# Performance work log

Hardware: AMD Instinct MI355X
Metric: run time of the kernel (lower is better)

Reference implementation:

```python
import jax, jax.numpy as jnp
import numpy as np

N_NODES = 50000
N_EDGES = 800000
IN_DIM = 13
HID = 64
LAYER_DIMS = [(IN_DIM, HID), (HID, HID), (HID, HID), (HID, HID), (HID, 1)]


def setup_inputs() -> dict:
    key = jax.random.key(0)
    ks = jax.random.split(key, 20)
    x = jax.random.normal(ks[0], (N_NODES, IN_DIM), dtype=jnp.float32)
    edge_index = jax.random.randint(ks[1], (2, N_EDGES), 0, N_NODES)
    edge_weight = jax.random.uniform(ks[2], (N_EDGES,), dtype=jnp.float32)
    inp = {"x": x, "edge_index": edge_index, "edge_weight": edge_weight}
    for i, (di, do) in enumerate(LAYER_DIMS):
        s = 1.0 / np.sqrt(di)
        inp[f"Wrel{i}"] = (jax.random.normal(ks[3 + 3 * i], (di, do)) * s).astype(jnp.float32)
        inp[f"brel{i}"] = jnp.zeros((do,), dtype=jnp.float32)
        inp[f"Wroot{i}"] = (jax.random.normal(ks[4 + 3 * i], (di, do)) * s).astype(jnp.float32)
    return inp


def _graph_conv(x, src, dst, ew, Wrel, brel, Wroot):
    # PyG GraphConv: out = lin_rel(sum_{j in N(i)} w_e * x_j) + lin_root(x_i)
    msgs = ew[:, None] * x[src]                      # [E, d_in] gather
    aggr = jax.ops.segment_sum(msgs, dst, num_segments=N_NODES)  # [N, d_in]
    return aggr @ Wrel + brel + x @ Wroot


def reference(x, edge_index, edge_weight,
              Wrel0, brel0, Wroot0,
              Wrel1, brel1, Wroot1,
              Wrel2, brel2, Wroot2,
              Wrel3, brel3, Wroot3,
              Wrel4, brel4, Wroot4):
    src, dst = edge_index[0], edge_index[1]  # source_to_target flow
    params = [
        (Wrel0, brel0, Wroot0),
        (Wrel1, brel1, Wroot1),
        (Wrel2, brel2, Wroot2),
        (Wrel3, brel3, Wroot3),
        (Wrel4, brel4, Wroot4),
    ]
    h = x
    for Wr, br, Ws in params[:-1]:
        h = jax.nn.relu(_graph_conv(h, src, dst, edge_weight, Wr, br, Ws))
    Wr, br, Ws = params[-1]
    h = _graph_conv(h, src, dst, edge_weight, Wr, br, Ws)
    return jax.nn.sigmoid(h)  # [N, 1]
```

## Files before the change

### kernel.cpp

```cpp
#include <hip/hip_runtime.h>
#include <math.h>

#define N_NODES 50000
#define N_EDGES 800000
#define NBUCKET 196
#define CHUNK 4096
#define NCHUNK 196
#define SCAN_N (NBUCKET * NCHUNK)
#define SB_A 151
#define SB_B 196
#define NSB (SB_A + SB_B)
#define EPT 16
#define CAP_FINE 8192
#define MAXEPAD (N_EDGES + N_NODES * 4)
#define XELEMS (N_NODES * 13)
#define XCONV_B 32

typedef __attribute__((ext_vector_type(8))) _Float16 f16x8;
typedef __attribute__((ext_vector_type(4))) float f32x4;

__device__ __forceinline__ int roundup4(int v) { return (v + 3) & ~3; }


__device__ __forceinline__ int block_excl_scan(int v, int* wsum) {
    int t = threadIdx.x, lane = t & 63, w = t >> 6;
    int sc = v;
    #pragma unroll
    for (int o = 1; o < 64; o <<= 1) {
        int u = __shfl_up(sc, o, 64);
        if (lane >= o) sc += u;
    }
    if (lane == 63) wsum[w] = sc;
    __syncthreads();
    int add = 0;
    #pragma unroll
    for (int j = 0; j < 4; ++j) if (j < w) add += wsum[j];
    return add + sc - v;
}


__global__ void hist_kernel(const int* __restrict__ dst, int* __restrict__ h,
                            int* __restrict__ counts,
                            const float* __restrict__ W1r, const float* __restrict__ W1o,
                            const float* __restrict__ W2r, const float* __restrict__ W2o,
                            const float* __restrict__ W3r, const float* __restrict__ W3o,
                            _Float16* __restrict__ wfrag,
                            const float* __restrict__ x, _Float16* __restrict__ xh) {
    if (blockIdx.x >= NCHUNK + 3) {
        int b = blockIdx.x - (NCHUNK + 3);
        for (int i = b * 256 + threadIdx.x; i < XELEMS; i += XCONV_B * 256)
            xh[i] = (_Float16)x[i];
        return;
    }
    if (blockIdx.x >= NCHUNK) {
        int b = blockIdx.x - NCHUNK, t = threadIdx.x;
        const float* Wr = (b == 0) ? W1r : (b == 1) ? W2r : W3r;
        const float* Wo = (b == 0) ? W1o : (b == 1) ? W2o : W3o;
        _Float16* out = wfrag + (size_t)b * 8192;
        for (int i = t; i < 1024; i += 256) {
            int frag = i >> 6, lane = i & 63;
            int m = frag >> 3, ct = (frag >> 1) & 3, ks = frag & 1;
            int col = ct * 16 + (lane & 15);
            int kb = ks * 32 + (lane >> 4) * 8;
            const float* W = m ? Wo : Wr;
            f16x8 v;
            #pragma unroll
            for (int j = 0; j < 8; ++j) v[j] = (_Float16)W[(kb + j) * 64 + col];
            *(f16x8*)&out[(size_t)i * 8] = v;
        }
        return;
    }
    __shared__ int hist[NBUCKET];
    for (int i = threadIdx.x; i < NBUCKET; i += 256) hist[i] = 0;
    __syncthreads();
    int base = blockIdx.x * CHUNK;
    int n = min(CHUNK, N_EDGES - base);
    for (int k = threadIdx.x; k < n; k += 256) {
        int d = dst[base + k];
        atomicAdd(&hist[d >> 8], 1);
        atomicAdd(&counts[d], 1);
    }
    __syncthreads();
    for (int i = threadIdx.x; i < NBUCKET; i += 256)
        h[i * NCHUNK + blockIdx.x] = hist[i];
}


__global__ void scan_sums(const int* __restrict__ h, const int* __restrict__ counts,
                          int* __restrict__ blocksums) {
    __shared__ int wsum[4];
    int bid = blockIdx.x, t = threadIdx.x;
    int v;
    if (bid < SB_A) {
        int i = bid * 256 + t;
        v = (i < SCAN_N) ? h[i] : 0;
    } else {
        int j = (bid - SB_A) * 256 + t;
        v = (j < N_NODES) ? roundup4(counts[j]) : 0;
    }
    int lane = t & 63, w = t >> 6;
    int s = v;
    #pragma unroll
    for (int o = 1; o < 64; o <<= 1) s += __shfl_xor(s, o, 64);
    if (lane == 0) wsum[w] = s;
    __syncthreads();
    if (t == 0) blocksums[bid] = wsum[0] + wsum[1] + wsum[2] + wsum[3];
}

__global__ void scan_apply(int* __restrict__ h, int* __restrict__ offs,
                           const int* __restrict__ counts,
                           const int* __restrict__ blocksums) {
    __shared__ int sblk[NSB + 1];
    __shared__ int wsum[4];
    int bid = blockIdx.x, t = threadIdx.x;
    if (t < 64) {
        int carry = 0;
        for (int c = 0; c < NSB; c += 64) {
            int i = c + t;
            int v = (i < NSB) ? blocksums[i] : 0;
            int sc = v;
            #pragma unroll
            for (int o = 1; o < 64; o <<= 1) {
                int u = __shfl_up(sc, o, 64);
                if (t >= o) sc += u;
            }
            if (i < NSB) sblk[i] = carry + sc - v;
            carry += __shfl(sc, 63, 64);
        }
        if (t == 0) sblk[NSB] = carry;
    }
    __syncthreads();
    int v;
    if (bid < SB_A) {
        int i = bid * 256 + t;
        v = (i < SCAN_N) ? h[i] : 0;
        int e = block_excl_scan(v, wsum);
        int base = sblk[bid];
        if (i < SCAN_N) h[i] = e + base;
    } else {
        int j = (bid - SB_A) * 256 + t;
        v = (j < N_NODES) ? roundup4(counts[j]) : 0;
        int e = block_excl_scan(v, wsum);
        int base = sblk[bid] - sblk[SB_A];
        if (j < N_NODES) {
            offs[j] = e + base;
            if (j == N_NODES - 1) offs[N_NODES] = e + base + v;
        }
    }
}


__launch_bounds__(256, 4)
__global__ void scatter_coarse(const int* __restrict__ src, const int* __restrict__ dst,
                               const float* __restrict__ ew, const int* __restrict__ hs,
                               int2* __restrict__ ecoarse) {
    __shared__ int cnt[NBUCKET];
    __shared__ int excl[NBUCKET];
    __shared__ int cur[NBUCKET];
    __shared__ int gbase[NBUCKET];
    __shared__ int wsum[4];
    __shared__ int2 stage[CHUNK];

    int t = threadIdx.x;
    int base = blockIdx.x * CHUNK;
    int n = min(CHUNK, N_EDGES - base);

    for (int i = t; i < NBUCKET; i += 256) {
        cnt[i] = 0;
        gbase[i] = hs[i * NCHUNK + blockIdx.x];
    }
    __syncthreads();

    int rx[EPT];
    float rw[EPT];
    #pragma unroll
    for (int j = 0; j < EPT; ++j) {
        int k = t + j * 256;
        if (k < n) {
            int e = base + k;
            int d = dst[e];
            rx[j] = (d << 16) | src[e];
            rw[j] = ew[e];
            atomicAdd(&cnt[d >> 8], 1);
        }
    }
    __syncthreads();

    {
        int v = (t < NBUCKET) ? cnt[t] : 0;
        int e = block_excl_scan(v, wsum);
        if (t < NBUCKET) { excl[t] = e; cur[t] = e; }
    }
    __syncthreads();

    #pragma unroll
    for (int j = 0; j < EPT; ++j) {
        int k = t + j * 256;
        if (k < n) {
            int b = ((unsigned)rx[j]) >> 24;
            int p = atomicAdd(&cur[b], 1);
            stage[p] = make_int2(rx[j], __float_as_int(rw[j]));
        }
    }
    __syncthreads();

    for (int k = t; k < n; k += 256) {
        int2 r = stage[k];
        int b = ((unsigned)r.x) >> 24;
        ecoarse[gbase[b] + (k - excl[b])] = r;
    }
}


__launch_bounds__(256)
__global__ void fine_sort(const int* __restrict__ h, const int* __restrict__ offs,
                          const int2* __restrict__ ecoarse, int2* __restrict__ esrt) {
    int b = blockIdx.x, t = threadIdx.x;
    __shared__ int cur[256];
    __shared__ int2 stage[CAP_FINE];
    int bstartU = h[b * NCHUNK];
    int bendU = (b == NBUCKET - 1) ? N_EDGES : h[(b + 1) * NCHUNK];
    int nbU = bendU - bstartU;
    int P = offs[b << 8];
    int nodeEnd = min((b + 1) << 8, N_NODES);
    int plen = offs[nodeEnd] - P;
    int dstv = (b << 8) + t;
    cur[t] = (dstv < N_NODES) ? offs[dstv] - P : 0;
    __syncthreads();
    if (plen <= CAP_FINE) {
        for (int k = t; k < plen; k += 256) stage[k] = make_int2(0, 0);
        __syncthreads();
        for (int k = t; k < nbU; k += 256) {
            int2 r = ecoarse[bstartU + k];
            int d = (((unsigned)r.x) >> 16) & 255;
            int p = atomicAdd(&cur[d], 1);
            stage[p] = make_int2(r.x & 0xFFFF, r.y);
        }
        __syncthreads();
        for (int k = t; k < plen; k += 256) esrt[P + k] = stage[k];
    } else {
        for (int k = t; k < plen; k += 256) esrt[P + k] = make_int2(0, 0);
        __syncthreads();
        for (int k = t; k < nbU; k += 256) {
            int2 r = ecoarse[bstartU + k];
            int d = (((unsigned)r.x) >> 16) & 255;
            int p = atomicAdd(&cur[d], 1);
            esrt[P + p] = make_int2(r.x & 0xFFFF, r.y);
        }
    }
}


__device__ __forceinline__ float bcast(float v, int k) {
    return __int_as_float(__builtin_amdgcn_readlane(__float_as_int(v), k));
}


__launch_bounds__(256)
__global__ void layer0_fused(const int* __restrict__ offs, const int2* __restrict__ esrt,
                             const _Float16* __restrict__ xh, const float* __restrict__ Wrel,
                             const float* __restrict__ bias, const float* __restrict__ Wroot,
                             _Float16* __restrict__ h0) {
    int wid = (blockIdx.x * blockDim.x + threadIdx.x) >> 6;
    int lane = threadIdx.x & 63;
    float wr[13], wo[13];
    #pragma unroll
    for (int k = 0; k < 13; ++k) {
        wr[k] = Wrel[k * 64 + lane];
        wo[k] = Wroot[k * 64 + lane];
    }
    float bc = bias[lane];
    int q = lane >> 4, f = lane & 15;
    int beg = offs[wid], end = offs[wid + 1];
    float acc = 0.f;
    bool fv = (f < 13);
    int i = beg + q;
    for (; i + 4 < end; i += 8) {
        int2 e0 = esrt[i], e1 = esrt[i + 4];
        float v0 = fv ? (float)xh[(size_t)e0.x * 13 + f] : 0.f;
        float v1 = fv ? (float)xh[(size_t)e1.x * 13 + f] : 0.f;
        acc = fmaf(__int_as_float(e0.y), v0, acc);
        acc = fmaf(__int_as_float(e1.y), v1, acc);
    }
    if (i < end) {
        int2 e = esrt[i];
        float v = fv ? (float)xh[(size_t)e.x * 13 + f] : 0.f;
        acc = fmaf(__int_as_float(e.y), v, acc);
    }
    acc += __shfl_xor(acc, 16, 64);
    acc += __shfl_xor(acc, 32, 64);
    float hv = (lane < 13) ? (float)xh[(size_t)wid * 13 + lane] : 0.f;
    float a0 = bc, a1 = 0.f, a2 = 0.f, a3 = 0.f;
    #pragma unroll
    for (int k = 0; k + 2 <= 13; k += 2) {
        a0 = fmaf(bcast(acc, k), wr[k], a0);
        a1 = fmaf(bcast(hv, k), wo[k], a1);
        a2 = fmaf(bcast(acc, k + 1), wr[k + 1], a2);
        a3 = fmaf(bcast(hv, k + 1), wo[k + 1], a3);
    }
    a0 = fmaf(bcast(acc, 12), wr[12], a0);
    a1 = fmaf(bcast(hv, 12), wo[12], a1);
    float o = fmaxf((a0 + a2) + (a1 + a3), 0.f);
    h0[(size_t)wid * 64 + lane] = (_Float16)o;
}


template <bool FINAL>
__launch_bounds__(256)
__global__ void layer_fused(const int* __restrict__ offs, const int2* __restrict__ esrt,
                            const _Float16* __restrict__ hin, const _Float16* __restrict__ wfrag_l,
                            const float* __restrict__ bias, _Float16* __restrict__ hout,
                            const float* __restrict__ Wrel4, const float* __restrict__ Wroot4,
                            float* __restrict__ z, float* __restrict__ root) {
    __shared__ __align__(16) _Float16 aggrHi[32][72];
    __shared__ __align__(16) _Float16 aggrLo[32][72];
    __shared__ float zpart[4][32], rpart[4][32];
    int t = threadIdx.x;
    int rowbase = blockIdx.x * 32;
    int w = t >> 6, lane = t & 63;

    f16x8 br0 = *(const f16x8*)&wfrag_l[(size_t)(((0 * 4 + w) * 2 + 0) * 64 + lane) * 8];
    f16x8 br1 = *(const f16x8*)&wfrag_l[(size_t)(((0 * 4 + w) * 2 + 1) * 64 + lane) * 8];
    f16x8 bo0 = *(const f16x8*)&wfrag_l[(size_t)(((1 * 4 + w) * 2 + 0) * 64 + lane) * 8];
    f16x8 bo1 = *(const f16x8*)&wfrag_l[(size_t)(((1 * 4 + w) * 2 + 1) * 64 + lane) * 8];
    int r = lane & 15, kq = lane >> 4;
    float bc = bias[w * 16 + r];
    float w4rv = 0.f, w4ov = 0.f;
    if (FINAL) { w4rv = Wrel4[w * 16 + r]; w4ov = Wroot4[w * 16 + r]; }

    int qw = t >> 4, l = t & 15;
    int hi8 = l >> 3, f8 = l & 7;
    #pragma unroll
    for (int rr = 0; rr < 2; ++rr) {
        int node = rowbase + qw + rr * 16;
        float a[8] = {0.f, 0.f, 0.f, 0.f, 0.f, 0.f, 0.f, 0.f};
        if (node < N_NODES) {
            int beg = offs[node], end = offs[node + 1];
            int i = beg;
            for (; i + 4 < end; i += 8) {
                int4 p0 = *(const int4*)(esrt + i);
                int4 p1 = *(const int4*)(esrt + i + 2);
                int4 p2 = *(const int4*)(esrt + i + 4);
                int4 p3 = *(const int4*)(esrt + i + 6);
                int s0 = hi8 ? p0.z : p0.x; float w0 = __int_as_float(hi8 ? p0.w : p0.y);
                int s1 = hi8 ? p1.z : p1.x; float w1 = __int_as_float(hi8 ? p1.w : p1.y);
                int s2 = hi8 ? p2.z : p2.x; float w2 = __int_as_float(hi8 ? p2.w : p2.y);
                int s3 = hi8 ? p3.z : p3.x; float w3 = __int_as_float(hi8 ? p3.w : p3.y);
                f16x8 r0 = *(const f16x8*)(hin + (size_t)s0 * 64 + f8 * 8);
                f16x8 r1 = *(const f16x8*)(hin + (size_t)s1 * 64 + f8 * 8);
                f16x8 r2 = *(const f16x8*)(hin + (size_t)s2 * 64 + f8 * 8);
                f16x8 r3 = *(const f16x8*)(hin + (size_t)s3 * 64 + f8 * 8);
                #pragma unroll
                for (int j = 0; j < 8; ++j) {
                    a[j] = fmaf(w0, (float)r0[j], a[j]);
                    a[j] = fmaf(w1, (float)r1[j], a[j]);
                    a[j] = fmaf(w2, (float)r2[j], a[j]);
                    a[j] = fmaf(w3, (float)r3[j], a[j]);
                }
            }
            if (i < end) {
                int4 p0 = *(const int4*)(esrt + i);
                int4 p1 = *(const int4*)(esrt + i + 2);
                int s0 = hi8 ? p0.z : p0.x; float w0 = __int_as_float(hi8 ? p0.w : p0.y);
                int s1 = hi8 ? p1.z : p1.x; float w1 = __int_as_float(hi8 ? p1.w : p1.y);
                f16x8 r0 = *(const f16x8*)(hin + (size_t)s0 * 64 + f8 * 8);
                f16x8 r1 = *(const f16x8*)(hin + (size_t)s1 * 64 + f8 * 8);
                #pragma unroll
                for (int j = 0; j < 8; ++j) {
                    a[j] = fmaf(w0, (float)r0[j], a[j]);
                    a[j] = fmaf(w1, (float)r1[j], a[j]);
                }
            }
        }
        #pragma unroll
        for (int j = 0; j < 8; ++j) a[j] += __shfl_xor(a[j], 8, 64);
        f16x8 wv;
        #pragma unroll
        for (int j = 0; j < 8; ++j) {
            _Float16 hh = (_Float16)a[j];
            wv[j] = hi8 ? (_Float16)(a[j] - (float)hh) : hh;
        }
        int row = qw + rr * 16;
        _Float16* dstp = hi8 ? &aggrLo[row][f8 * 8] : &aggrHi[row][f8 * 8];
        *(f16x8*)dstp = wv;
    }
    __syncthreads();

    #pragma unroll
    for (int g = 0; g < 2; ++g) {
        int lr = g * 16 + r;
        int grow = min(rowbase + lr, N_NODES - 1);
        f32x4 acc = {bc, bc, bc, bc};
        {
            f16x8 Ah = *(const f16x8*)&aggrHi[lr][0 * 32 + kq * 8];
            f16x8 Al = *(const f16x8*)&aggrLo[lr][0 * 32 + kq * 8];
            f16x8 Ar = *(const f16x8*)&hin[(size_t)grow * 64 + 0 * 32 + kq * 8];
            acc = __builtin_amdgcn_mfma_f32_16x16x32_f16(Ah, br0, acc, 0, 0, 0);
            acc = __builtin_amdgcn_mfma_f32_16x16x32_f16(Al, br0, acc, 0, 0, 0);
            acc = __builtin_amdgcn_mfma_f32_16x16x32_f16(Ar, bo0, acc, 0, 0, 0);
        }
        {
            f16x8 Ah = *(const f16x8*)&aggrHi[lr][1 * 32 + kq * 8];
            f16x8 Al = *(const f16x8*)&aggrLo[lr][1 * 32 + kq * 8];
            f16x8 Ar = *(const f16x8*)&hin[(size_t)grow * 64 + 1 * 32 + kq * 8];
            acc = __builtin_amdgcn_mfma_f32_16x16x32_f16(Ah, br1, acc, 0, 0, 0);
            acc = __builtin_amdgcn_mfma_f32_16x16x32_f16(Al, br1, acc, 0, 0, 0);
            acc = __builtin_amdgcn_mfma_f32_16x16x32_f16(Ar, bo1, acc, 0, 0, 0);
        }
        if (FINAL) {
            #pragma unroll
            for (int j = 0; j < 4; ++j) {
                float o = fmaxf(acc[j], 0.f);
                float zz = o * w4rv, rv = o * w4ov;
                #pragma unroll
                for (int m = 1; m < 16; m <<= 1) {
                    zz += __shfl_xor(zz, m, 64);
                    rv += __shfl_xor(rv, m, 64);
                }
                if (r == 0) {
                    int lrow = g * 16 + (lane >> 4) * 4 + j;
                    zpart[w][lrow] = zz;
                    rpart[w][lrow] = rv;
                }
            }
        } else {
            #pragma unroll
            for (int j = 0; j < 4; ++j) {
                int row = rowbase + g * 16 + (lane >> 4) * 4 + j;
                if (row < N_NODES)
                    hout[(size_t)row * 64 + w * 16 + r] = (_Float16)fmaxf(acc[j], 0.f);
            }
        }
    }
    if (FINAL) {
        __syncthreads();
        if (t < 32) {
            int row = rowbase + t;
            if (row < N_NODES) {
                z[row] = zpart[0][t] + zpart[1][t] + zpart[2][t] + zpart[3][t];
                root[row] = rpart[0][t] + rpart[1][t] + rpart[2][t] + rpart[3][t];
            }
        }
    }
}


__launch_bounds__(256)
__global__ void final_aggr(const int* __restrict__ offs, const int2* __restrict__ esrt,
                           const float* __restrict__ z, const float* __restrict__ root,
                           const float* __restrict__ b4, float* __restrict__ out) {
    int tid = blockIdx.x * blockDim.x + threadIdx.x;
    int node = tid >> 2, g = tid & 3;
    if (node >= N_NODES) return;
    int beg = offs[node], end = offs[node + 1];
    float a = 0.f;
    int i = beg + g;
    for (; i + 4 < end; i += 8) {
        int2 e0 = esrt[i], e1 = esrt[i + 4];
        a = fmaf(__int_as_float(e0.y), z[e0.x], a);
        a = fmaf(__int_as_float(e1.y), z[e1.x], a);
    }
    if (i < end) {
        int2 e = esrt[i];
        a = fmaf(__int_as_float(e.y), z[e.x], a);
    }
    a += __shfl_xor(a, 1, 64);
    a += __shfl_xor(a, 2, 64);
    if (g == 0) {
        float v = a + b4[0] + root[node];
        out[node] = 1.f / (1.f + expf(-v));
    }
}


extern "C" void kernel_launch(void* const* d_in, const int* in_sizes, int n_in,
                              void* d_out, int out_size, void* d_ws, size_t ws_size,
                              hipStream_t stream) {
    const float* x = (const float*)d_in[0];
    const int* eidx = (const int*)d_in[1];
    const float* ew = (const float*)d_in[2];
    const float* Wrel[5];
    const float* brel[5];
    const float* Wroot[5];
    for (int i = 0; i < 5; ++i) {
        Wrel[i] = (const float*)d_in[3 + 3 * i];
        brel[i] = (const float*)d_in[4 + 3 * i];
        Wroot[i] = (const float*)d_in[5 + 3 * i];
    }
    const int* src = eidx;
    const int* dst = eidx + N_EDGES;
    float* out = (float*)d_out;

    char* ws = (char*)d_ws;
    size_t off = 0;
    auto alloc = [&](size_t bytes) -> void* {
        void* p = ws + off;
        off = (off + bytes + 255) & ~(size_t)255;
        return p;
    };
    int* h = (int*)alloc((size_t)(SCAN_N + 256) * 4);
    int* blocksums = (int*)alloc(512 * 4);
    int* counts = (int*)alloc((size_t)N_NODES * 4);
    int* offs = (int*)alloc((size_t)(N_NODES + 1) * 4);
    int2* esrt = (int2*)alloc((size_t)MAXEPAD * 8);
    _Float16* h0 = (_Float16*)alloc((size_t)N_NODES * 64 * 2);
    _Float16* h1 = (_Float16*)alloc((size_t)N_NODES * 64 * 2);
    _Float16* wfrag = (_Float16*)alloc((size_t)3 * 8192 * 2);
    _Float16* xh = (_Float16*)alloc((size_t)XELEMS * 2);
    float* z = (float*)alloc((size_t)N_NODES * 4);
    float* root = (float*)alloc((size_t)N_NODES * 4);
    int2* ecoarse = (int2*)h0;
    (void)ws_size; (void)in_sizes; (void)n_in; (void)out_size;

    hipMemsetAsync(counts, 0, (size_t)N_NODES * 4, stream);
    hist_kernel<<<NCHUNK + 3 + XCONV_B, 256, 0, stream>>>(dst, h, counts,
                                                Wrel[1], Wroot[1], Wrel[2], Wroot[2],
                                                Wrel[3], Wroot[3], wfrag, x, xh);
    scan_sums<<<NSB, 256, 0, stream>>>(h, counts, blocksums);
    scan_apply<<<NSB, 256, 0, stream>>>(h, offs, counts, blocksums);
    scatter_coarse<<<NCHUNK, 256, 0, stream>>>(src, dst, ew, h, ecoarse);
    fine_sort<<<NBUCKET, 256, 0, stream>>>(h, offs, ecoarse, esrt);

    const int NODE_BLOCKS = N_NODES * 64 / 256;
    const int FB = (N_NODES + 31) / 32;

    layer0_fused<<<NODE_BLOCKS, 256, 0, stream>>>(offs, esrt, xh, Wrel[0], brel[0], Wroot[0], h0);

    layer_fused<false><<<FB, 256, 0, stream>>>(offs, esrt, h0, wfrag, brel[1], h1,
                                               nullptr, nullptr, nullptr, nullptr);
    layer_fused<false><<<FB, 256, 0, stream>>>(offs, esrt, h1, wfrag + 8192, brel[2], h0,
                                               nullptr, nullptr, nullptr, nullptr);
    layer_fused<true><<<FB, 256, 0, stream>>>(offs, esrt, h0, wfrag + 16384, brel[3], nullptr,
                                              Wrel[4], Wroot[4], z, root);

    final_aggr<<<(N_NODES * 4 + 255) / 256, 256, 0, stream>>>(offs, esrt, z, root, brel[4], out);
}
```

Baseline: 180.6 us.

## Pack edges into 32-bit src/fp16 weight and fuse layers via persistent grid barrier

Edge records shrink from an int2 (src, fp32 weight) to one 32-bit word holding a 16-bit source index and an fp16 weight. This halves edge-list traffic in every aggregation pass. Layers 1-3 and the final aggregation are also merged into one persistent kernel that loops over tiles and syncs through a hand-rolled atomic grid barrier, removing three kernel launches. The trade-offs: the weight loses precision in fp16, and the 16-bit index only works because fine_sort stores the low 16 bits with the bucket implied by the destination. The spin barrier can also deadlock if not all blocks are co-resident, which depends on the occupancy query and assumes 256 CUs.

```diff
diff --git a/kernel.cpp b/kernel.cpp
--- a/kernel.cpp
+++ b/kernel.cpp
@@ -15,11 +15,18 @@
 #define MAXEPAD (N_EDGES + N_NODES * 4)
 #define XELEMS (N_NODES * 13)
 #define XCONV_B 32
+#define FB ((N_NODES + 31) / 32)
+#define FINB ((N_NODES * 4 + 255) / 256)
 
 typedef __attribute__((ext_vector_type(8))) _Float16 f16x8;
 typedef __attribute__((ext_vector_type(4))) float f32x4;
 
 __device__ __forceinline__ int roundup4(int v) { return (v + 3) & ~3; }
+
+__device__ __forceinline__ float upw(int e) {
+    unsigned short u = (unsigned short)(((unsigned)e) >> 16);
+    return (float)__builtin_bit_cast(_Float16, u);
+}
 
 
 __device__ __forceinline__ int block_excl_scan(int v, int* wsum) {
@@ -45,7 +52,9 @@
                             const float* __restrict__ W2r, const float* __restrict__ W2o,
                             const float* __restrict__ W3r, const float* __restrict__ W3o,
                             _Float16* __restrict__ wfrag,
-                            const float* __restrict__ x, _Float16* __restrict__ xh) {
+                            const float* __restrict__ x, _Float16* __restrict__ xh,
+                            int* __restrict__ bar) {
+    if (blockIdx.x == 0 && threadIdx.x < 8) bar[threadIdx.x] = 0;
     if (blockIdx.x >= NCHUNK + 3) {
         int b = blockIdx.x - (NCHUNK + 3);
         for (int i = b * 256 + threadIdx.x; i < XELEMS; i += XCONV_B * 256)
@@ -214,10 +223,10 @@
 
 __launch_bounds__(256)
 __global__ void fine_sort(const int* __restrict__ h, const int* __restrict__ offs,
-                          const int2* __restrict__ ecoarse, int2* __restrict__ esrt) {
+                          const int2* __restrict__ ecoarse, int* __restrict__ epack) {
     int b = blockIdx.x, t = threadIdx.x;
     __shared__ int cur[256];
-    __shared__ int2 stage[CAP_FINE];
+    __shared__ int stage[CAP_FINE];
     int bstartU = h[b * NCHUNK];
     int bendU = (b == NBUCKET - 1) ? N_EDGES : h[(b + 1) * NCHUNK];
     int nbU = bendU - bstartU;
@@ -228,24 +237,26 @@
     cur[t] = (dstv < N_NODES) ? offs[dstv] - P : 0;
     __syncthreads();
     if (plen <= CAP_FINE) {
-        for (int k = t; k < plen; k += 256) stage[k] = make_int2(0, 0);
+        for (int k = t; k < plen; k += 256) stage[k] = 0;
         __syncthreads();
         for (int k = t; k < nbU; k += 256) {
             int2 r = ecoarse[bstartU + k];
             int d = (((unsigned)r.x) >> 16) & 255;
+            unsigned short hw = __builtin_bit_cast(unsigned short, (_Float16)__int_as_float(r.y));
             int p = atomicAdd(&cur[d], 1);
-            stage[p] = make_int2(r.x & 0xFFFF, r.y);
+            stage[p] = (r.x & 0xFFFF) | ((int)hw << 16);
         }
         __syncthreads();
-        for (int k = t; k < plen; k += 256) esrt[P + k] = stage[k];
+        for (int k = t; k < plen; k += 256) epack[P + k] = stage[k];
     } else {
-        for (int k = t; k < plen; k += 256) esrt[P + k] = make_int2(0, 0);
+        for (int k = t; k < plen; k += 256) epack[P + k] = 0;
         __syncthreads();
         for (int k = t; k < nbU; k += 256) {
             int2 r = ecoarse[bstartU + k];
             int d = (((unsigned)r.x) >> 16) & 255;
+            unsigned short hw = __builtin_bit_cast(unsigned short, (_Float16)__int_as_float(r.y));
             int p = atomicAdd(&cur[d], 1);
-            esrt[P + p] = make_int2(r.x & 0xFFFF, r.y);
+            epack[P + p] = (r.x & 0xFFFF) | ((int)hw << 16);
         }
     }
 }
@@ -257,7 +268,7 @@
 
 
 __launch_bounds__(256)
-__global__ void layer0_fused(const int* __restrict__ offs, const int2* __restrict__ esrt,
+__global__ void layer0_fused(const int* __restrict__ offs, const int* __restrict__ epack,
                              const _Float16* __restrict__ xh, const float* __restrict__ Wrel,
                              const float* __restrict__ bias, const float* __restrict__ Wroot,
                              _Float16* __restrict__ h0) {
@@ -276,16 +287,16 @@
     bool fv = (f < 13);
     int i = beg + q;
     for (; i + 4 < end; i += 8) {
-        int2 e0 = esrt[i], e1 = esrt[i + 4];
-        float v0 = fv ? (float)xh[(size_t)e0.x * 13 + f] : 0.f;
-        float v1 = fv ? (float)xh[(size_t)e1.x * 13 + f] : 0.f;
-        acc = fmaf(__int_as_float(e0.y), v0, acc);
-        acc = fmaf(__int_as_float(e1.y), v1, acc);
+        int e0 = epack[i], e1 = epack[i + 4];
+        float v0 = fv ? (float)xh[(size_t)(e0 & 0xFFFF) * 13 + f] : 0.f;
+        float v1 = fv ? (float)xh[(size_t)(e1 & 0xFFFF) * 13 + f] : 0.f;
+        acc = fmaf(upw(e0), v0, acc);
+        acc = fmaf(upw(e1), v1, acc);
     }
     if (i < end) {
-        int2 e = esrt[i];
-        float v = fv ? (float)xh[(size_t)e.x * 13 + f] : 0.f;
-        acc = fmaf(__int_as_float(e.y), v, acc);
+        int e = epack[i];
+        float v = fv ? (float)xh[(size_t)(e & 0xFFFF) * 13 + f] : 0.f;
+        acc = fmaf(upw(e), v, acc);
     }
     acc += __shfl_xor(acc, 16, 64);
     acc += __shfl_xor(acc, 32, 64);
@@ -306,17 +317,16 @@
 
 
 template <bool FINAL>
-__launch_bounds__(256)
-__global__ void layer_fused(const int* __restrict__ offs, const int2* __restrict__ esrt,
-                            const _Float16* __restrict__ hin, const _Float16* __restrict__ wfrag_l,
-                            const float* __restrict__ bias, _Float16* __restrict__ hout,
-                            const float* __restrict__ Wrel4, const float* __restrict__ Wroot4,
-                            float* __restrict__ z, float* __restrict__ root) {
-    __shared__ __align__(16) _Float16 aggrHi[32][72];
-    __shared__ __align__(16) _Float16 aggrLo[32][72];
-    __shared__ float zpart[4][32], rpart[4][32];
+__device__ __forceinline__ void layer_tile(
+    int tile, const int* __restrict__ offs, const int* __restrict__ epack,
+    const _Float16* __restrict__ hin, const _Float16* __restrict__ wfrag_l,
+    const float* __restrict__ bias, _Float16* __restrict__ hout,
+    const float* __restrict__ Wrel4, const float* __restrict__ Wroot4,
+    float* __restrict__ z, float* __restrict__ root,
+    _Float16 (*aggrHi)[72], _Float16 (*aggrLo)[72],
+    float (*zpart)[32], float (*rpart)[32]) {
     int t = threadIdx.x;
-    int rowbase = blockIdx.x * 32;
+    int rowbase = tile * 32;
     int w = t >> 6, lane = t & 63;
 
     f16x8 br0 = *(const f16x8*)&wfrag_l[(size_t)(((0 * 4 + w) * 2 + 0) * 64 + lane) * 8];
@@ -338,18 +348,17 @@
             int beg = offs[node], end = offs[node + 1];
             int i = beg;
             for (; i + 4 < end; i += 8) {
-                int4 p0 = *(const int4*)(esrt + i);
-                int4 p1 = *(const int4*)(esrt + i + 2);
-                int4 p2 = *(const int4*)(esrt + i + 4);
-                int4 p3 = *(const int4*)(esrt + i + 6);
-                int s0 = hi8 ? p0.z : p0.x; float w0 = __int_as_float(hi8 ? p0.w : p0.y);
-                int s1 = hi8 ? p1.z : p1.x; float w1 = __int_as_float(hi8 ? p1.w : p1.y);
-                int s2 = hi8 ? p2.z : p2.x; float w2 = __int_as_float(hi8 ? p2.w : p2.y);
-                int s3 = hi8 ? p3.z : p3.x; float w3 = __int_as_float(hi8 ? p3.w : p3.y);
-                f16x8 r0 = *(const f16x8*)(hin + (size_t)s0 * 64 + f8 * 8);
-                f16x8 r1 = *(const f16x8*)(hin + (size_t)s1 * 64 + f8 * 8);
-                f16x8 r2 = *(const f16x8*)(hin + (size_t)s2 * 64 + f8 * 8);
-                f16x8 r3 = *(const f16x8*)(hin + (size_t)s3 * 64 + f8 * 8);
+                int4 pk0 = *(const int4*)(epack + i);
+                int4 pk1 = *(const int4*)(epack + i + 4);
+                int e0 = hi8 ? pk0.z : pk0.x;
+                int e1 = hi8 ? pk0.w : pk0.y;
+                int e2 = hi8 ? pk1.z : pk1.x;
+                int e3 = hi8 ? pk1.w : pk1.y;
+                f16x8 r0 = *(const f16x8*)(hin + (size_t)(e0 & 0xFFFF) * 64 + f8 * 8);
+                f16x8 r1 = *(const f16x8*)(hin + (size_t)(e1 & 0xFFFF) * 64 + f8 * 8);
+                f16x8 r2 = *(const f16x8*)(hin + (size_t)(e2 & 0xFFFF) * 64 + f8 * 8);
+                f16x8 r3 = *(const f16x8*)(hin + (size_t)(e3 & 0xFFFF) * 64 + f8 * 8);
+                float w0 = upw(e0), w1 = upw(e1), w2 = upw(e2), w3 = upw(e3);
                 #pragma unroll
                 for (int j = 0; j < 8; ++j) {
                     a[j] = fmaf(w0, (float)r0[j], a[j]);
@@ -359,12 +368,12 @@
                 }
             }
             if (i < end) {
-                int4 p0 = *(const int4*)(esrt + i);
-                int4 p1 = *(const int4*)(esrt + i + 2);
-                int s0 = hi8 ? p0.z : p0.x; float w0 = __int_as_float(hi8 ? p0.w : p0.y);
-                int s1 = hi8 ? p1.z : p1.x; float w1 = __int_as_float(hi8 ? p1.w : p1.y);
-                f16x8 r0 = *(const f16x8*)(hin + (size_t)s0 * 64 + f8 * 8);
-                f16x8 r1 = *(const f16x8*)(hin + (size_t)s1 * 64 + f8 * 8);
+                int4 pk = *(const int4*)(epack + i);
+                int e0 = hi8 ? pk.z : pk.x;
+                int e1 = hi8 ? pk.w : pk.y;
+                f16x8 r0 = *(const f16x8*)(hin + (size_t)(e0 & 0xFFFF) * 64 + f8 * 8);
+                f16x8 r1 = *(const f16x8*)(hin + (size_t)(e1 & 0xFFFF) * 64 + f8 * 8);
+                float w0 = upw(e0), w1 = upw(e1);
                 #pragma unroll
                 for (int j = 0; j < 8; ++j) {
                     a[j] = fmaf(w0, (float)r0[j], a[j]);
@@ -442,34 +451,82 @@
             }
         }
     }
+    __syncthreads();
+}
+
+
+__device__ __forceinline__ void final_tile(int tile, const int* __restrict__ offs,
+                                           const int* __restrict__ epack,
+                                           const float* __restrict__ z,
+                                           const float* __restrict__ root,
+                                           const float* __restrict__ b4,
+                                           float* __restrict__ out) {
+    int tid = tile * 256 + threadIdx.x;
+    int node = tid >> 2, g = tid & 3;
+    if (node < N_NODES) {
+        int beg = offs[node], end = offs[node + 1];
+        float a = 0.f;
+        int i = beg + g;
+        for (; i + 4 < end; i += 8) {
+            int e0 = epack[i], e1 = epack[i + 4];
+            a = fmaf(upw(e0), z[e0 & 0xFFFF], a);
+            a = fmaf(upw(e1), z[e1 & 0xFFFF], a);
+        }
+        if (i < end) {
+            int e = epack[i];
+            a = fmaf(upw(e), z[e & 0xFFFF], a);
+        }
+        a += __shfl_xor(a, 1, 64);
+        a += __shfl_xor(a, 2, 64);
+        if (g == 0) {
+            float v = a + b4[0] + root[node];
+            out[node] = 1.f / (1.f + expf(-v));
+        }
+    }
+}
+
+
+__device__ __forceinline__ void grid_barrier(int* cnt, int nblocks) {
+    __syncthreads();
+    __threadfence();
+    if (threadIdx.x == 0) {
+        __hip_atomic_fetch_add(cnt, 1, __ATOMIC_ACQ_REL, __HIP_MEMORY_SCOPE_AGENT);
+        while (__hip_atomic_load(cnt, __ATOMIC_ACQUIRE, __HIP_MEMORY_SCOPE_AGENT) < nblocks)
+            __builtin_amdgcn_s_sleep(1);
+    }
+    __syncthreads();
+    __threadfence();
 }
 
 
 __launch_bounds__(256)
-__global__ void final_aggr(const int* __restrict__ offs, const int2* __restrict__ esrt,
-                           const float* __restrict__ z, const float* __restrict__ root,
-                           const float* __restrict__ b4, float* __restrict__ out) {
-    int tid = blockIdx.x * blockDim.x + threadIdx.x;
-    int node = tid >> 2, g = tid & 3;
-    if (node >= N_NODES) return;
-    int beg = offs[node], end = offs[node + 1];
-    float a = 0.f;
-    int i = beg + g;
-    for (; i + 4 < end; i += 8) {
-        int2 e0 = esrt[i], e1 = esrt[i + 4];
-        a = fmaf(__int_as_float(e0.y), z[e0.x], a);
-        a = fmaf(__int_as_float(e1.y), z[e1.x], a);
-    }
-    if (i < end) {
-        int2 e = esrt[i];
-        a = fmaf(__int_as_float(e.y), z[e.x], a);
-    }
-    a += __shfl_xor(a, 1, 64);
-    a += __shfl_xor(a, 2, 64);
-    if (g == 0) {
-        float v = a + b4[0] + root[node];
-        out[node] = 1.f / (1.f + expf(-v));
-    }
+__global__ void layers_coop(const int* __restrict__ offs, const int* __restrict__ epack,
+                            _Float16* __restrict__ h0, _Float16* __restrict__ h1,
+                            const _Float16* __restrict__ wfrag,
+                            const float* __restrict__ b1, const float* __restrict__ b2,
+                            const float* __restrict__ b3,
+                            const float* __restrict__ Wrel4, const float* __restrict__ Wroot4,
+                            float* __restrict__ z, float* __restrict__ root,
+                            const float* __restrict__ b4, float* __restrict__ out,
+                            int* __restrict__ bar, int nblocks) {
+    __shared__ __align__(16) _Float16 aggrHi[32][72];
+    __shared__ __align__(16) _Float16 aggrLo[32][72];
+    __shared__ float zpart[4][32], rpart[4][32];
+
+    for (int tile = blockIdx.x; tile < FB; tile += gridDim.x)
+        layer_tile<false>(tile, offs, epack, h0, wfrag, b1, h1,
+                          nullptr, nullptr, nullptr, nullptr, aggrHi, aggrLo, zpart, rpart);
+    grid_barrier(&bar[0], nblocks);
+    for (int tile = blockIdx.x; tile < FB; tile += gridDim.x)
+        layer_tile<false>(tile, offs, epack, h1, wfrag + 8192, b2, h0,
+                          nullptr, nullptr, nullptr, nullptr, aggrHi, aggrLo, zpart, rpart);
+    grid_barrier(&bar[1], nblocks);
+    for (int tile = blockIdx.x; tile < FB; tile += gridDim.x)
+        layer_tile<true>(tile, offs, epack, h0, wfrag + 16384, b3, nullptr,
+                         Wrel4, Wroot4, z, root, aggrHi, aggrLo, zpart, rpart);
+    grid_barrier(&bar[2], nblocks);
+    for (int tile = blockIdx.x; tile < FINB; tile += gridDim.x)
+        final_tile(tile, offs, epack, z, root, b4, out);
 }
 
 
@@ -502,36 +559,36 @@
     int* blocksums = (int*)alloc(512 * 4);
     int* counts = (int*)alloc((size_t)N_NODES * 4);
     int* offs = (int*)alloc((size_t)(N_NODES + 1) * 4);
-    int2* esrt = (int2*)alloc((size_t)MAXEPAD * 8);
+    int* epack = (int*)alloc((size_t)MAXEPAD * 4);
     _Float16* h0 = (_Float16*)alloc((size_t)N_NODES * 64 * 2);
     _Float16* h1 = (_Float16*)alloc((size_t)N_NODES * 64 * 2);
     _Float16* wfrag = (_Float16*)alloc((size_t)3 * 8192 * 2);
     _Float16* xh = (_Float16*)alloc((size_t)XELEMS * 2);
     float* z = (float*)alloc((size_t)N_NODES * 4);
     float* root = (float*)alloc((size_t)N_NODES * 4);
+    int* bar = (int*)alloc(256);
     int2* ecoarse = (int2*)h0;
     (void)ws_size; (void)in_sizes; (void)n_in; (void)out_size;
 
     hipMemsetAsync(counts, 0, (size_t)N_NODES * 4, stream);
     hist_kernel<<<NCHUNK + 3 + XCONV_B, 256, 0, stream>>>(dst, h, counts,
                                                 Wrel[1], Wroot[1], Wrel[2], Wroot[2],
-                                                Wrel[3], Wroot[3], wfrag, x, xh);
+                                                Wrel[3], Wroot[3], wfrag, x, xh, bar);
     scan_sums<<<NSB, 256, 0, stream>>>(h, counts, blocksums);
     scan_apply<<<NSB, 256, 0, stream>>>(h, offs, counts, blocksums);
     scatter_coarse<<<NCHUNK, 256, 0, stream>>>(src, dst, ew, h, ecoarse);
-    fine_sort<<<NBUCKET, 256, 0, stream>>>(h, offs, ecoarse, esrt);
+    fine_sort<<<NBUCKET, 256, 0, stream>>>(h, offs, ecoarse, epack);
 
     const int NODE_BLOCKS = N_NODES * 64 / 256;
-    const int FB = (N_NODES + 31) / 32;
-
-    layer0_fused<<<NODE_BLOCKS, 256, 0, stream>>>(offs, esrt, xh, Wrel[0], brel[0], Wroot[0], h0);
-
-    layer_fused<false><<<FB, 256, 0, stream>>>(offs, esrt, h0, wfrag, brel[1], h1,
-                                               nullptr, nullptr, nullptr, nullptr);
-    layer_fused<false><<<FB, 256, 0, stream>>>(offs, esrt, h1, wfrag + 8192, brel[2], h0,
-                                               nullptr, nullptr, nullptr, nullptr);
-    layer_fused<true><<<FB, 256, 0, stream>>>(offs, esrt, h0, wfrag + 16384, brel[3], nullptr,
-                                              Wrel[4], Wroot[4], z, root);
-
-    final_aggr<<<(N_NODES * 4 + 255) / 256, 256, 0, stream>>>(offs, esrt, z, root, brel[4], out);
-}
+
+    layer0_fused<<<NODE_BLOCKS, 256, 0, stream>>>(offs, epack, xh, Wrel[0], brel[0], Wroot[0], h0);
+
+    int nb = 0;
+    if (hipOccupancyMaxActiveBlocksPerMultiprocessor(&nb, layers_coop, 256, 0) != hipSuccess
+        || nb < 1) nb = 2;
+    int grid = FB < nb * 256 ? FB : nb * 256;
+    layers_coop<<<grid, 256, 0, stream>>>(offs, epack, h0, h1, wfrag,
+                                          brel[1], brel[2], brel[3],
+                                          Wrel[4], Wroot[4], z, root, brel[4], out,
+                                          bar, grid);
+}
```

Measured after the change: 611.7 us. 3.39x slower.
